# Kernel optimization log

Hardware: AMD Instinct MI355X
Metric: run time of the kernel (lower is better)

## Reference

```python
import jax, jax.numpy as jnp
import numpy as np

B, S, D = 4, 1024, 1280
K = 4            # projector_pool_stride
IN = D * K       # 5120
H = 2048         # projector_hidden_dim
O = 2048         # llm_dim
E = 4            # num_experts
TOPK = 2         # num_experts_per_tok
EPS_RMS = 1e-8
EPS_W = 1e-6


def setup_inputs() -> dict:
    key = jax.random.key(0)
    ks = jax.random.split(key, 16)
    g = lambda i, shape, scale: jax.random.normal(ks[i], shape, jnp.float32) * scale
    return {
        "x": jax.random.normal(ks[0], (B, S, D), jnp.float32),
        "conv_w": g(1, (D, 1, 3), 0.1),            # depthwise conv kernel (O, I/g, W)
        "conv_b": jnp.zeros((D,), jnp.float32),
        "rms_w": jnp.ones((IN,), jnp.float32),
        "router_w": g(2, (E, IN), 0.02),
        "sw1": g(3, (H, IN), 0.02), "sb1": jnp.zeros((H,), jnp.float32),
        "sw2": g(4, (O, H), 0.01),  "sb2": jnp.zeros((O,), jnp.float32),
        "ew1": g(5, (E, H, IN), 0.02), "eb1": jnp.zeros((E, H), jnp.float32),
        "ew2": g(6, (E, O, H), 0.01),  "eb2": jnp.zeros((E, O), jnp.float32),
    }


def reference(x, conv_w, conv_b, rms_w, router_w, sw1, sb1, sw2, sb2, ew1, eb1, ew2, eb2):
    b, s, d = x.shape
    # depthwise temporal conv (groups = channels), residual add
    xc = jnp.transpose(x, (0, 2, 1))  # [B, D, S]
    xc = jax.lax.conv_general_dilated(
        xc, conv_w, window_strides=(1,), padding=[(1, 1)],
        dimension_numbers=("NCH", "OIH", "NCH"), feature_group_count=d)
    xc = xc + conv_b[None, :, None]
    x = x + jnp.transpose(xc, (0, 2, 1))
    # pad seq to multiple of K, then fold K frames into channel dim
    pad = (-s) % K
    if pad:
        x = jnp.pad(x, ((0, 0), (0, pad), (0, 0)))
    t = x.shape[1] // K
    x = x.reshape(b, t, d * K)  # [B, T, IN]
    # LlamaRMSNorm in fp32
    xf = x.astype(jnp.float32)
    n = xf * jax.lax.rsqrt(jnp.mean(xf * xf, axis=-1, keepdims=True) + EPS_RMS)
    n = (rms_w * n).astype(x.dtype)
    # shared expert: 2-layer ReLU MLP
    shared = jnp.maximum(n @ sw1.T + sb1, 0.0) @ sw2.T + sb2  # [B, T, O]
    # sigmoid router + top-k
    flat = n.reshape(-1, n.shape[-1])  # [Tk, IN]
    router_logits = flat @ router_w.T  # [Tk, E]
    router_probs = jax.nn.sigmoid(router_logits)
    scores, idx = jax.lax.top_k(router_probs, TOPK)
    w = scores / (jnp.sum(scores, axis=-1, keepdims=True) + EPS_W)
    w = w.astype(flat.dtype)
    # combine weights [Tk, E]: zero for unrouted experts == loop's skipped/masked tokens
    combine = jnp.sum(jax.nn.one_hot(idx, E, dtype=flat.dtype) * w[..., None], axis=1)
    # dense expert evaluation weighted by combine (math-equivalent to gather/scatter loop)
    h = jnp.maximum(jnp.einsum("td,ehd->teh", flat, ew1) + eb1, 0.0)  # [Tk, E, H]
    oe = jnp.einsum("teh,eoh->teo", h, ew2) + eb2                       # [Tk, E, O]
    routed = jnp.einsum("teo,te->to", oe, combine).reshape(b, t, -1)
    return shared + routed
```

## Files before the change

### kernel.cpp

```cpp
#include <hip/hip_runtime.h>

typedef __attribute__((ext_vector_type(8))) short short8v;
typedef __attribute__((ext_vector_type(4))) float floatx4;

#define IND 5120

static __device__ __forceinline__ short f2bf(float f) {
    unsigned int u = __builtin_bit_cast(unsigned int, f);
    unsigned int r = (u + 0x7FFFu + ((u >> 16) & 1u)) >> 16;
    return (short)r;
}

__global__ __launch_bounds__(256)
void pre_kernel(const float* __restrict__ x, const float* __restrict__ conv_w,
                const float* __restrict__ conv_b, const float* __restrict__ rms_w,
                const float* __restrict__ router_w,
                short* __restrict__ nbf, float* __restrict__ combine)
{
    __shared__ float xs[6 * 1280];
    __shared__ float cw[3 * 1280];
    __shared__ float cb[1280];
    __shared__ float red[8];
    __shared__ float rred[16];

    const int t  = blockIdx.x;
    const int b  = t >> 8;
    const int tt = t & 255;
    const int s0 = tt * 4;
    const int tid = threadIdx.x;

    for (int idx = tid; idx < 7680; idx += 256) {
        int f = idx / 1280, d = idx - f * 1280;
        int s = s0 - 1 + f;
        float v = 0.f;
        if (s >= 0 && s < 1024) v = x[((size_t)b * 1024 + s) * 1280 + d];
        xs[idx] = v;
    }
    for (int idx = tid; idx < 3840; idx += 256) cw[idx] = conv_w[idx];
    for (int idx = tid; idx < 1280; idx += 256) cb[idx] = conv_b[idx];
    __syncthreads();

    float yv[20];
    float ss = 0.f;
#pragma unroll
    for (int j = 0; j < 20; ++j) {
        int k = tid + j * 256;
        int f = k / 1280, d = k - f * 1280;
        float xm = xs[(f + 1) * 1280 + d];
        float y = xm + xs[f * 1280 + d] * cw[d * 3 + 0]
                     + xm               * cw[d * 3 + 1]
                     + xs[(f + 2) * 1280 + d] * cw[d * 3 + 2]
                     + cb[d];
        yv[j] = y;
        ss += y * y;
    }
    const int lane = tid & 63, wid = tid >> 6;
#pragma unroll
    for (int off = 32; off; off >>= 1) ss += __shfl_xor(ss, off);
    if (lane == 0) red[wid] = ss;
    __syncthreads();
    if (tid == 0) {
        float s4 = red[0] + red[1] + red[2] + red[3];
        red[4] = 1.0f / sqrtf(s4 * (1.0f / 5120.f) + 1e-8f);
    }
    __syncthreads();
    const float inv = red[4];

    const size_t rowbase = (size_t)(t >> 7) * 80 * 8192 + (size_t)(t & 127) * 64;
    const int xr = (t & 7) << 3;

    float r0 = 0.f, r1 = 0.f, r2 = 0.f, r3 = 0.f;
#pragma unroll
    for (int j = 0; j < 20; ++j) {
        int k = tid + j * 256;
        float nv = yv[j] * inv * rms_w[k];
        nbf[rowbase + (size_t)(k >> 6) * 8192 + ((k & 63) ^ xr)] = f2bf(nv);
        r0 += nv * router_w[k];
        r1 += nv * router_w[IND + k];
        r2 += nv * router_w[2 * IND + k];
        r3 += nv * router_w[3 * IND + k];
    }
#pragma unroll
    for (int off = 32; off; off >>= 1) {
        r0 += __shfl_xor(r0, off); r1 += __shfl_xor(r1, off);
        r2 += __shfl_xor(r2, off); r3 += __shfl_xor(r3, off);
    }
    if (lane == 0) { rred[wid*4+0]=r0; rred[wid*4+1]=r1; rred[wid*4+2]=r2; rred[wid*4+3]=r3; }
    __syncthreads();
    if (tid == 0) {
        float p[4];
#pragma unroll
        for (int e = 0; e < 4; ++e) {
            float lg = rred[e] + rred[4+e] + rred[8+e] + rred[12+e];
            p[e] = 1.0f / (1.0f + expf(-lg));
        }
        int i1 = 0;
        for (int e = 1; e < 4; ++e) if (p[e] > p[i1]) i1 = e;
        int i2 = (i1 == 0) ? 1 : 0;
        for (int e = 0; e < 4; ++e) if (e != i1 && p[e] > p[i2]) i2 = e;
        float wsum = p[i1] + p[i2] + 1e-6f;
        float c[4] = {0.f, 0.f, 0.f, 0.f};
        c[i1] = p[i1] / wsum;
        c[i2] = p[i2] / wsum;
        combine[t*4+0] = c[0]; combine[t*4+1] = c[1];
        combine[t*4+2] = c[2]; combine[t*4+3] = c[3];
    }
}

__global__ __launch_bounds__(256)
void convert_tiled(const float* __restrict__ src, short* __restrict__ dst,
                   int C, int KT, int row_toff, int k_toff)
{
    const int bx = blockIdx.x;
    const int by = blockIdx.y;
    short* tbase = dst + ((size_t)(by + row_toff) * KT + (bx + k_toff)) * 8192;
    const float* sbase = src + (size_t)by * 128 * C + (size_t)bx * 64;
#pragma unroll
    for (int it = 0; it < 4; ++it) {
        const int idx = it * 256 + threadIdx.x;
        const int r = idx >> 3, ch = idx & 7;
        const float* s = sbase + (size_t)r * C + ch * 8;
        float4 a = *(const float4*)s;
        float4 b = *(const float4*)(s + 4);
        short8v o;
        o[0] = f2bf(a.x); o[1] = f2bf(a.y); o[2] = f2bf(a.z); o[3] = f2bf(a.w);
        o[4] = f2bf(b.x); o[5] = f2bf(b.y); o[6] = f2bf(b.z); o[7] = f2bf(b.w);
        *(short8v*)(tbase + r * 64 + ((ch ^ (r & 7)) << 3)) = o;
    }
}

template<int MODE>
__global__ __launch_bounds__(256, 5)
void gemm_kernel(const short* __restrict__ A, const short* __restrict__ Bw,
                 const float* __restrict__ sb1, const float* __restrict__ eb1,
                 const float* __restrict__ combine,
                 short* __restrict__ Hout, float* __restrict__ Pout)
{
    constexpr int KT  = (MODE == 1) ? 80 : 160;
    constexpr int NKT = (MODE == 1) ? 80 : 40;
    __shared__ short As[8192];
    __shared__ short Bs[8192];
    const int tid  = threadIdx.x;
    const int lane = tid & 63;
    const int wid  = tid >> 6;
    const int wr   = wid >> 1, wc = wid & 1;
    const int kt0  = (MODE == 2) ? blockIdx.z * NKT : 0;

    const short* at = A  + ((size_t)blockIdx.y * KT + kt0) * 8192;
    const short* bt = Bw + ((size_t)blockIdx.x * KT + kt0) * 8192;

    floatx4 acc[4][4] = {};

    for (int kt = 0; kt < NKT; ++kt) {
#pragma unroll
        for (int i = 0; i < 4; ++i) {
            const int o = (i * 256 + tid) * 8;
            __builtin_amdgcn_global_load_lds(
                (const __attribute__((address_space(1))) void*)(at + o),
                (__attribute__((address_space(3))) void*)(As + o), 16, 0, 0);
            __builtin_amdgcn_global_load_lds(
                (const __attribute__((address_space(1))) void*)(bt + o),
                (__attribute__((address_space(3))) void*)(Bs + o), 16, 0, 0);
        }
        at += 8192; bt += 8192;
        __syncthreads();
#pragma unroll
        for (int kk = 0; kk < 2; ++kk) {
            short8v af[4], bfr[4];
#pragma unroll
            for (int m = 0; m < 4; ++m) {
                const int r = wr * 64 + m * 16 + (lane & 15);
                const int c = (kk * 32 + (lane >> 4) * 8) ^ ((r & 7) << 3);
                af[m] = *(const short8v*)(As + r * 64 + c);
            }
#pragma unroll
            for (int n = 0; n < 4; ++n) {
                const int r = wc * 64 + n * 16 + (lane & 15);
                const int c = (kk * 32 + (lane >> 4) * 8) ^ ((r & 7) << 3);
                bfr[n] = *(const short8v*)(Bs + r * 64 + c);
            }
#pragma unroll
            for (int m = 0; m < 4; ++m)
#pragma unroll
                for (int n = 0; n < 4; ++n)
                    acc[m][n] = __builtin_amdgcn_mfma_f32_16x16x32_bf16(
                        af[m], bfr[n], acc[m][n], 0, 0, 0);
        }
        __syncthreads();
    }

    const int m0 = blockIdx.y * 128;
    const int n0 = blockIdx.x * 128;
#pragma unroll
    for (int m = 0; m < 4; ++m) {
        const int rb = m0 + wr * 64 + m * 16 + ((lane >> 4) * 4);
#pragma unroll
        for (int n = 0; n < 4; ++n) {
            const int col = n0 + wc * 64 + n * 16 + (lane & 15);
#pragma unroll
            for (int r = 0; r < 4; ++r) {
                const int rowg = rb + r;
                float v = acc[m][n][r];
                if constexpr (MODE == 1) {
                    v += (col < 2048) ? sb1[col] : eb1[col - 2048];
                    v = fmaxf(v, 0.0f);
                    if (col >= 2048) v *= combine[rowg * 4 + ((col - 2048) >> 11)];
                    const size_t tb = ((size_t)(rowg >> 7) * 160 + (col >> 6)) * 8192;
                    Hout[tb + (size_t)(rowg & 127) * 64 + ((col & 63) ^ ((rowg & 7) << 3))] = f2bf(v);
                } else {
                    float* P = Pout + (size_t)blockIdx.z * (1024u * 2048u);
                    P[(size_t)rowg * 2048 + col] = v;
                }
            }
        }
    }
}

__global__ __launch_bounds__(256)
void reduce_kernel(const float* __restrict__ part, const float* __restrict__ sb2,
                   const float* __restrict__ eb2, const float* __restrict__ combine,
                   float* __restrict__ out)
{
    const int idx  = blockIdx.x * 256 + threadIdx.x;
    const int base = idx * 4;
    const int row  = base >> 11;
    const int col  = base & 2047;
    const size_t NP = 1024u * 2048u;
    float4 s0 = *(const float4*)(part + base);
    float4 s1 = *(const float4*)(part + NP + base);
    float4 s2 = *(const float4*)(part + 2 * NP + base);
    float4 s3 = *(const float4*)(part + 3 * NP + base);
    const float c0 = combine[row * 4 + 0], c1 = combine[row * 4 + 1];
    const float c2 = combine[row * 4 + 2], c3 = combine[row * 4 + 3];
    float4 o;
    float* op = (float*)&o;
    const float* p0 = (const float*)&s0; const float* p1 = (const float*)&s1;
    const float* p2 = (const float*)&s2; const float* p3 = (const float*)&s3;
#pragma unroll
    for (int j = 0; j < 4; ++j) {
        const int c = col + j;
        float b2 = sb2[c] + c0 * eb2[c] + c1 * eb2[2048 + c]
                 + c2 * eb2[4096 + c] + c3 * eb2[6144 + c];
        op[j] = p0[j] + p1[j] + p2[j] + p3[j] + b2;
    }
    *(float4*)(out + base) = o;
}

extern "C" void kernel_launch(void* const* d_in, const int* in_sizes, int n_in,
                              void* d_out, int out_size, void* d_ws, size_t ws_size,
                              hipStream_t stream)
{
    const float* x        = (const float*)d_in[0];
    const float* conv_w   = (const float*)d_in[1];
    const float* conv_b   = (const float*)d_in[2];
    const float* rms_w    = (const float*)d_in[3];
    const float* router_w = (const float*)d_in[4];
    const float* sw1      = (const float*)d_in[5];
    const float* sb1      = (const float*)d_in[6];
    const float* sw2      = (const float*)d_in[7];
    const float* sb2      = (const float*)d_in[8];
    const float* ew1      = (const float*)d_in[9];
    const float* eb1      = (const float*)d_in[10];
    const float* ew2      = (const float*)d_in[11];
    const float* eb2      = (const float*)d_in[12];
    float* out = (float*)d_out;

    char* ws = (char*)d_ws;
    short* nbf     = (short*)(ws);
    short* hbf     = (short*)(ws + 10485760);
    short* w1b     = (short*)(ws + 31457280);
    float* part2   = (float*)(ws + 31457280);
    short* w2b     = (short*)(ws + 136314880);
    float* combine = (float*)(ws + 178257920);

    pre_kernel<<<1024, 256, 0, stream>>>(x, conv_w, conv_b, rms_w, router_w, nbf, combine);

    convert_tiled<<<dim3(80, 16), 256, 0, stream>>>(sw1, w1b, 5120, 80, 0, 0);
    convert_tiled<<<dim3(80, 64), 256, 0, stream>>>(ew1, w1b, 5120, 80, 16, 0);
    convert_tiled<<<dim3(32, 16), 256, 0, stream>>>(sw2, w2b, 2048, 160, 0, 0);
    for (int e = 0; e < 4; ++e)
        convert_tiled<<<dim3(32, 16), 256, 0, stream>>>(
            ew2 + (size_t)e * 2048 * 2048, w2b, 2048, 160, 0, 32 + e * 32);

    gemm_kernel<1><<<dim3(80, 8), 256, 0, stream>>>(
        nbf, w1b, sb1, eb1, combine, hbf, nullptr);
    gemm_kernel<2><<<dim3(16, 8, 4), 256, 0, stream>>>(
        hbf, w2b, nullptr, nullptr, combine, nullptr, part2);

    reduce_kernel<<<2048, 256, 0, stream>>>(part2, sb2, eb2, combine, out);
}
```

Baseline: 595.4 us.

## Fuse fp32-to-bf16 weight conversion into GEMM B-tile staging

Removes the separate weight conversion kernels and has both GEMMs load fp32 weights directly, converting to bf16 with packed cvt instructions while writing swizzled LDS tiles. This avoids writing and rereading a converted bf16 weight copy. In exchange, each M-block reads fp32 weights (twice the bytes) through synchronous register loads instead of async global-to-LDS loads, and occupancy bound is lowered.

```diff
diff --git a/kernel.cpp b/kernel.cpp
--- a/kernel.cpp
+++ b/kernel.cpp
@@ -107,62 +107,54 @@
     }
 }
 
-__global__ __launch_bounds__(256)
-void convert_tiled(const float* __restrict__ src, short* __restrict__ dst,
-                   int C, int KT, int row_toff, int k_toff)
-{
-    const int bx = blockIdx.x;
-    const int by = blockIdx.y;
-    short* tbase = dst + ((size_t)(by + row_toff) * KT + (bx + k_toff)) * 8192;
-    const float* sbase = src + (size_t)by * 128 * C + (size_t)bx * 64;
-#pragma unroll
-    for (int it = 0; it < 4; ++it) {
-        const int idx = it * 256 + threadIdx.x;
-        const int r = idx >> 3, ch = idx & 7;
-        const float* s = sbase + (size_t)r * C + ch * 8;
-        float4 a = *(const float4*)s;
-        float4 b = *(const float4*)(s + 4);
-        short8v o;
-        o[0] = f2bf(a.x); o[1] = f2bf(a.y); o[2] = f2bf(a.z); o[3] = f2bf(a.w);
-        o[4] = f2bf(b.x); o[5] = f2bf(b.y); o[6] = f2bf(b.z); o[7] = f2bf(b.w);
-        *(short8v*)(tbase + r * 64 + ((ch ^ (r & 7)) << 3)) = o;
-    }
-}
-
-template<int MODE>
-__global__ __launch_bounds__(256, 5)
-void gemm_kernel(const short* __restrict__ A, const short* __restrict__ Bw,
-                 const float* __restrict__ sb1, const float* __restrict__ eb1,
-                 const float* __restrict__ combine,
-                 short* __restrict__ Hout, float* __restrict__ Pout)
-{
-    constexpr int KT  = (MODE == 1) ? 80 : 160;
-    constexpr int NKT = (MODE == 1) ? 80 : 40;
+static __device__ __forceinline__ void stage_b_fp32(
+    const float* __restrict__ bsrc, int ldb, short* __restrict__ Bs, int tid)
+{
+#pragma unroll
+    for (int i = 0; i < 8; ++i) {
+        const int g   = i * 256 + tid;
+        const int row = g >> 4;
+        const int cg  = g & 15;
+        float4 v = *(const float4*)(bsrc + (size_t)row * ldb + cg * 4);
+        unsigned int u0, u1;
+        asm("v_cvt_pk_bf16_f32 %0, %1, %2" : "=v"(u0) : "v"(v.x), "v"(v.y));
+        asm("v_cvt_pk_bf16_f32 %0, %1, %2" : "=v"(u1) : "v"(v.z), "v"(v.w));
+        const int off = row * 64 + ((cg * 4) ^ ((row & 7) << 3));
+        uint2 w; w.x = u0; w.y = u1;
+        *(uint2*)(Bs + off) = w;
+    }
+}
+
+__global__ __launch_bounds__(256, 2)
+void fc1_gemm(const short* __restrict__ A, const float* __restrict__ sw1,
+              const float* __restrict__ ew1, const float* __restrict__ sb1,
+              const float* __restrict__ eb1, const float* __restrict__ combine,
+              short* __restrict__ Hout)
+{
     __shared__ short As[8192];
     __shared__ short Bs[8192];
     const int tid  = threadIdx.x;
     const int lane = tid & 63;
     const int wid  = tid >> 6;
     const int wr   = wid >> 1, wc = wid & 1;
-    const int kt0  = (MODE == 2) ? blockIdx.z * NKT : 0;
-
-    const short* at = A  + ((size_t)blockIdx.y * KT + kt0) * 8192;
-    const short* bt = Bw + ((size_t)blockIdx.x * KT + kt0) * 8192;
+    const int n0   = blockIdx.x * 128;
+
+    const float* bsrc = (n0 < 2048) ? (sw1 + (size_t)n0 * 5120)
+                                    : (ew1 + (size_t)(n0 - 2048) * 5120);
+    const short* at = A + (size_t)blockIdx.y * 80 * 8192;
 
     floatx4 acc[4][4] = {};
 
-    for (int kt = 0; kt < NKT; ++kt) {
+    for (int kt = 0; kt < 80; ++kt) {
 #pragma unroll
         for (int i = 0; i < 4; ++i) {
             const int o = (i * 256 + tid) * 8;
             __builtin_amdgcn_global_load_lds(
                 (const __attribute__((address_space(1))) void*)(at + o),
                 (__attribute__((address_space(3))) void*)(As + o), 16, 0, 0);
-            __builtin_amdgcn_global_load_lds(
-                (const __attribute__((address_space(1))) void*)(bt + o),
-                (__attribute__((address_space(3))) void*)(Bs + o), 16, 0, 0);
-        }
-        at += 8192; bt += 8192;
+        }
+        stage_b_fp32(bsrc + kt * 64, 5120, Bs, tid);
+        at += 8192;
         __syncthreads();
 #pragma unroll
         for (int kk = 0; kk < 2; ++kk) {
@@ -190,7 +182,6 @@
     }
 
     const int m0 = blockIdx.y * 128;
-    const int n0 = blockIdx.x * 128;
 #pragma unroll
     for (int m = 0; m < 4; ++m) {
         const int rb = m0 + wr * 64 + m * 16 + ((lane >> 4) * 4);
@@ -201,17 +192,84 @@
             for (int r = 0; r < 4; ++r) {
                 const int rowg = rb + r;
                 float v = acc[m][n][r];
-                if constexpr (MODE == 1) {
-                    v += (col < 2048) ? sb1[col] : eb1[col - 2048];
-                    v = fmaxf(v, 0.0f);
-                    if (col >= 2048) v *= combine[rowg * 4 + ((col - 2048) >> 11)];
-                    const size_t tb = ((size_t)(rowg >> 7) * 160 + (col >> 6)) * 8192;
-                    Hout[tb + (size_t)(rowg & 127) * 64 + ((col & 63) ^ ((rowg & 7) << 3))] = f2bf(v);
-                } else {
-                    float* P = Pout + (size_t)blockIdx.z * (1024u * 2048u);
-                    P[(size_t)rowg * 2048 + col] = v;
-                }
-            }
+                v += (col < 2048) ? sb1[col] : eb1[col - 2048];
+                v = fmaxf(v, 0.0f);
+                if (col >= 2048) v *= combine[rowg * 4 + ((col - 2048) >> 11)];
+                const size_t tb = ((size_t)(rowg >> 7) * 160 + (col >> 6)) * 8192;
+                Hout[tb + (size_t)(rowg & 127) * 64 + ((col & 63) ^ ((rowg & 7) << 3))] = f2bf(v);
+            }
+        }
+    }
+}
+
+__global__ __launch_bounds__(256, 2)
+void fc2_gemm(const short* __restrict__ A, const float* __restrict__ sw2,
+              const float* __restrict__ ew2, float* __restrict__ Pout)
+{
+    __shared__ short As[8192];
+    __shared__ short Bs[8192];
+    const int tid  = threadIdx.x;
+    const int lane = tid & 63;
+    const int wid  = tid >> 6;
+    const int wr   = wid >> 1, wc = wid & 1;
+    const int n0   = blockIdx.x * 128;
+
+    const short* at = A + ((size_t)blockIdx.y * 160 + blockIdx.z * 40) * 8192;
+
+    floatx4 acc[4][4] = {};
+
+    for (int kt = 0; kt < 40; ++kt) {
+#pragma unroll
+        for (int i = 0; i < 4; ++i) {
+            const int o = (i * 256 + tid) * 8;
+            __builtin_amdgcn_global_load_lds(
+                (const __attribute__((address_space(1))) void*)(at + o),
+                (__attribute__((address_space(3))) void*)(As + o), 16, 0, 0);
+        }
+        const int kk = (blockIdx.z * 40 + kt) << 6;
+        const float* bsrc = (kk < 2048)
+            ? (sw2 + kk)
+            : (ew2 + (size_t)((kk >> 11) - 1) * 4194304 + (kk & 2047));
+        bsrc += (size_t)n0 * 2048;
+        stage_b_fp32(bsrc, 2048, Bs, tid);
+        at += 8192;
+        __syncthreads();
+#pragma unroll
+        for (int kq = 0; kq < 2; ++kq) {
+            short8v af[4], bfr[4];
+#pragma unroll
+            for (int m = 0; m < 4; ++m) {
+                const int r = wr * 64 + m * 16 + (lane & 15);
+                const int c = (kq * 32 + (lane >> 4) * 8) ^ ((r & 7) << 3);
+                af[m] = *(const short8v*)(As + r * 64 + c);
+            }
+#pragma unroll
+            for (int n = 0; n < 4; ++n) {
+                const int r = wc * 64 + n * 16 + (lane & 15);
+                const int c = (kq * 32 + (lane >> 4) * 8) ^ ((r & 7) << 3);
+                bfr[n] = *(const short8v*)(Bs + r * 64 + c);
+            }
+#pragma unroll
+            for (int m = 0; m < 4; ++m)
+#pragma unroll
+                for (int n = 0; n < 4; ++n)
+                    acc[m][n] = __builtin_amdgcn_mfma_f32_16x16x32_bf16(
+                        af[m], bfr[n], acc[m][n], 0, 0, 0);
+        }
+        __syncthreads();
+    }
+
+    const int m0 = blockIdx.y * 128;
+    float* P = Pout + (size_t)blockIdx.z * (1024u * 2048u);
+#pragma unroll
+    for (int m = 0; m < 4; ++m) {
+        const int rb = m0 + wr * 64 + m * 16 + ((lane >> 4) * 4);
+#pragma unroll
+        for (int n = 0; n < 4; ++n) {
+            const int col = n0 + wc * 64 + n * 16 + (lane & 15);
+#pragma unroll
+            for (int r = 0; r < 4; ++r)
+                P[(size_t)(rb + r) * 2048 + col] = acc[m][n][r];
         }
     }
 }
@@ -268,24 +326,15 @@
     char* ws = (char*)d_ws;
     short* nbf     = (short*)(ws);
     short* hbf     = (short*)(ws + 10485760);
-    short* w1b     = (short*)(ws + 31457280);
     float* part2   = (float*)(ws + 31457280);
-    short* w2b     = (short*)(ws + 136314880);
-    float* combine = (float*)(ws + 178257920);
+    float* combine = (float*)(ws + 65011712);
 
     pre_kernel<<<1024, 256, 0, stream>>>(x, conv_w, conv_b, rms_w, router_w, nbf, combine);
 
-    convert_tiled<<<dim3(80, 16), 256, 0, stream>>>(sw1, w1b, 5120, 80, 0, 0);
-    convert_tiled<<<dim3(80, 64), 256, 0, stream>>>(ew1, w1b, 5120, 80, 16, 0);
-    convert_tiled<<<dim3(32, 16), 256, 0, stream>>>(sw2, w2b, 2048, 160, 0, 0);
-    for (int e = 0; e < 4; ++e)
-        convert_tiled<<<dim3(32, 16), 256, 0, stream>>>(
-            ew2 + (size_t)e * 2048 * 2048, w2b, 2048, 160, 0, 32 + e * 32);
-
-    gemm_kernel<1><<<dim3(80, 8), 256, 0, stream>>>(
-        nbf, w1b, sb1, eb1, combine, hbf, nullptr);
-    gemm_kernel<2><<<dim3(16, 8, 4), 256, 0, stream>>>(
-        hbf, w2b, nullptr, nullptr, combine, nullptr, part2);
+    fc1_gemm<<<dim3(80, 8), 256, 0, stream>>>(
+        nbf, sw1, ew1, sb1, eb1, combine, hbf);
+    fc2_gemm<<<dim3(16, 8, 4), 256, 0, stream>>>(
+        hbf, sw2, ew2, part2);
 
     reduce_kernel<<<2048, 256, 0, stream>>>(part2, sb2, eb2, combine, out);
 }
```

Result: slower. 690.0 us (+15.9%).
